# Performance work log

Measured on AMD Instinct MI355X. Metric: run time of the kernel, lower is better.

The kernel has to match this reference:

```python
import jax, jax.numpy as jnp
import numpy as np

DROPOUT_P = 0.0  # undefined global `dropout_p` in source; pinned to 0 (identity) for determinism


def setup_inputs() -> dict:
    key = jax.random.key(0)
    k1, k2, k3 = jax.random.split(key, 3)
    B, Lq, Lk, D = 16, 4096, 4096, 64
    return {
        "query": jax.random.normal(k1, (B, Lq, D), dtype=jnp.float32),
        "key": jax.random.normal(k2, (B, Lk, D), dtype=jnp.float32),
        "value": jax.random.normal(k3, (B, Lk, D), dtype=jnp.float32),
        "scale_factor": jnp.ones((1,), dtype=jnp.float32),
    }


def reference(query, key, value, scale_factor):
    # scores: [B, Lq, Lk] -- the large HBM-materialized intermediate
    scores = jnp.einsum("bqd,bkd->bqk", query, key) / scale_factor
    probs = jax.nn.softmax(scores, axis=-1)
    # dropout with p = DROPOUT_P = 0.0 is the identity
    out = jnp.einsum("bqk,bkd->bqd", probs, value)
    return out
```

## Files before the change

### kernel.cpp

```cpp
#include <hip/hip_runtime.h>
#include <hip/hip_fp16.h>

typedef _Float16 half2_t __attribute__((ext_vector_type(2)));
typedef _Float16 half4_t __attribute__((ext_vector_type(4)));
typedef _Float16 half8_t __attribute__((ext_vector_type(8)));
typedef float   float4_t __attribute__((ext_vector_type(4)));
typedef float  float16_t __attribute__((ext_vector_type(16)));

static __device__ __forceinline__ half2_t cvt_pk(float a, float b) {
    return __builtin_bit_cast(half2_t, __builtin_amdgcn_cvt_pkrtz(a, b));
}
static __device__ __forceinline__ half4_t cvt_pk4(float a, float b, float c, float d) {
    half2_t lo = cvt_pk(a, b), hi = cvt_pk(c, d);
    half4_t r;
    r[0] = lo[0]; r[1] = lo[1]; r[2] = hi[0]; r[3] = hi[1];
    return r;
}
static __device__ __forceinline__ half8_t cvt_pk8(const float4& a, const float4& b) {
    half4_t lo = cvt_pk4(a.x, a.y, a.z, a.w);
    half4_t hi = cvt_pk4(b.x, b.y, b.z, b.w);
    return __builtin_shufflevector(lo, hi, 0, 1, 2, 3, 4, 5, 6, 7);
}
static __device__ __forceinline__ half8_t join8(half4_t lo, half4_t hi) {
    return __builtin_shufflevector(lo, hi, 0, 1, 2, 3, 4, 5, 6, 7);
}
static __device__ __forceinline__ float f3(float a, float b, float c) {
    return fmaxf(fmaxf(a, b), c);
}

namespace {
constexpr int kB       = 16;
constexpr int kL       = 4096;
constexpr int kD       = 64;
constexpr int kQTile   = 128;
constexpr int kBK      = 64;
constexpr int kTiles   = kL / kBK;
constexpr int kSplit   = 2;
constexpr int kTilesHf = kTiles / kSplit;
constexpr int kTileH   = kBK * kD;
constexpr int kKStride = 72;
constexpr size_t kWsHalves = (size_t)kB * kTiles * kTileH;
constexpr size_t kOHalves  = (size_t)kB * kL * kD;
}


__global__ __launch_bounds__(256) void prep_kv(const float* __restrict__ K,
                                               const float* __restrict__ V,
                                               _Float16* __restrict__ Kws,
                                               _Float16* __restrict__ Vws)
{
    int blk = blockIdx.x;
    const int tid = threadIdx.x;
    if (blk < kB * kTiles) {
        const float* src = K + (size_t)blk * kTileH;
        _Float16* dst = Kws + (size_t)blk * kTileH;
#pragma unroll
        for (int i = 0; i < 2; ++i) {
            const int task = tid + 256 * i;
            const int row  = task >> 3;
            const int g    = task & 7;
            const int srow = (row & ~12) | ((row & 4) << 1) | ((row & 8) >> 1);
            const float* p = src + srow * kD + g * 8;
            const float4 a  = *(const float4*)p;
            const float4 b2 = *(const float4*)(p + 4);
            *(half8_t*)(dst + task * 8) = cvt_pk8(a, b2);
        }
    } else {
        blk -= kB * kTiles;
        const float* src = V + (size_t)blk * kTileH;
        _Float16* dst = Vws + (size_t)blk * kTileH;
        const int d  = tid & 63;
        const int vw = tid >> 6;
#pragma unroll
        for (int i = 0; i < 2; ++i) {
            const int c8 = vw * 2 + i;
            const int k0 = c8 * 8;
            float p[8];
#pragma unroll
            for (int j = 0; j < 8; ++j) p[j] = src[(k0 + j) * kD + d];
            half4_t lo = cvt_pk4(p[0], p[1], p[2], p[3]);
            half4_t hi = cvt_pk4(p[4], p[5], p[6], p[7]);
            *(half8_t*)(dst + (c8 * 64 + d) * 8) = join8(lo, hi);
        }
    }
}

__global__ __launch_bounds__(256, 4)
void fa_fwd(const float* __restrict__ Q, const _Float16* __restrict__ Kws,
            const _Float16* __restrict__ Vws, const float* __restrict__ scale_ptr,
            float* __restrict__ Out, _Float16* __restrict__ O2ws,
            float* __restrict__ Mlws)
{
    __shared__ __align__(16) _Float16 Ksh[2][kBK * kKStride];

    const int tid  = threadIdx.x;
    const int wave = tid >> 6;
    const int lane = tid & 63;
    const int l31  = lane & 31;
    const int hi   = lane >> 5;

    const int b  = blockIdx.y;
    const int hf = blockIdx.z;
    const int q0 = blockIdx.x * kQTile + wave * 32;

    const int task0 = tid, task1 = tid + 256;
    const int koff0 = (task0 >> 3) * kKStride + (task0 & 7) * 8;
    const int koff1 = (task1 >> 3) * kKStride + (task1 & 7) * 8;

    const float qscale = 1.4426950408889634f / scale_ptr[0];

    const float*    Qb = Q   + (size_t)b * kL * kD;
    const _Float16* Kt = Kws + ((size_t)b * kTiles + (size_t)hf * kTilesHf) * kTileH;
    const _Float16* Vt = Vws + ((size_t)b * kTiles + (size_t)hf * kTilesHf) * kTileH;

    half8_t qfrag[4];
    {
        const float* qrow = Qb + (size_t)(q0 + l31) * kD;
#pragma unroll
        for (int kd = 0; kd < 4; ++kd) {
            const float* p = qrow + kd * 16 + hi * 8;
            half8_t h;
#pragma unroll
            for (int j = 0; j < 8; ++j) h[j] = (_Float16)(p[j] * qscale);
            qfrag[kd] = h;
        }
    }

    float16_t O[2];
    O[0] = (float16_t)0.0f;
    O[1] = (float16_t)0.0f;
    float m_run = -__builtin_inff();
    float l_run = 0.0f;
    const float16_t Zc = (float16_t)0.0f;

    half8_t kp[2];
    kp[0] = *(const half8_t*)(Kt + task0 * 8);
    kp[1] = *(const half8_t*)(Kt + task1 * 8);
    *(half8_t*)(&Ksh[0][koff0]) = kp[0];
    *(half8_t*)(&Ksh[0][koff1]) = kp[1];
    kp[0] = *(const half8_t*)(Kt + (size_t)kTileH + task0 * 8);
    kp[1] = *(const half8_t*)(Kt + (size_t)kTileH + task1 * 8);
    __syncthreads();

    for (int t = 0; t < kTilesHf; ++t) {
        const int cur = t & 1;
        const _Float16* Kb = Ksh[cur];
        _Float16* Kn = Ksh[cur ^ 1];

        const _Float16* vtile = Vt + (size_t)t * kTileH;
        half8_t vr0[4], vr1[4];
#pragma unroll
        for (int kb = 0; kb < 4; ++kb) {
            const _Float16* pch = vtile + (kb * 2 + hi) * 512;
            vr0[kb] = *(const half8_t*)(pch + l31 * 8);
            vr1[kb] = *(const half8_t*)(pch + (32 + l31) * 8);
        }

        float16_t S0, S1;
        {
            half8_t kf0, kf1;
            kf0 = *(const half8_t*)(&Kb[(l31)      * kKStride + 0 * 16 + hi * 8]);
            kf1 = *(const half8_t*)(&Kb[(32 + l31) * kKStride + 0 * 16 + hi * 8]);
            __builtin_amdgcn_s_setprio(1);
            S0 = __builtin_amdgcn_mfma_f32_32x32x16_f16(kf0, qfrag[0], Zc, 0, 0, 0);
            S1 = __builtin_amdgcn_mfma_f32_32x32x16_f16(kf1, qfrag[0], Zc, 0, 0, 0);
#pragma unroll
            for (int kd = 1; kd < 4; ++kd) {
                kf0 = *(const half8_t*)(&Kb[(l31)      * kKStride + kd * 16 + hi * 8]);
                kf1 = *(const half8_t*)(&Kb[(32 + l31) * kKStride + kd * 16 + hi * 8]);
                S0 = __builtin_amdgcn_mfma_f32_32x32x16_f16(kf0, qfrag[kd], S0, 0, 0, 0);
                S1 = __builtin_amdgcn_mfma_f32_32x32x16_f16(kf1, qfrag[kd], S1, 0, 0, 0);
            }
            __builtin_amdgcn_s_setprio(0);
        }

        *(half8_t*)(&Kn[koff0]) = kp[0];
        *(half8_t*)(&Kn[koff1]) = kp[1];
        {
            const int nt = (t + 2) & (kTilesHf - 1);
            const _Float16* kn = Kt + (size_t)nt * kTileH;
            kp[0] = *(const half8_t*)(kn + task0 * 8);
            kp[1] = *(const half8_t*)(kn + task1 * 8);
        }

        float v0 = f3(S0[0],  S0[1],  S0[2]);
        float v1 = f3(S0[3],  S0[4],  S0[5]);
        float v2 = f3(S0[6],  S0[7],  S0[8]);
        float v3 = f3(S0[9],  S0[10], S0[11]);
        float v4 = f3(S0[12], S0[13], S0[14]);
        float v5 = f3(S0[15], S1[0],  S1[1]);
        float v6 = f3(S1[2],  S1[3],  S1[4]);
        float v7 = f3(S1[5],  S1[6],  S1[7]);
        float v8 = f3(S1[8],  S1[9],  S1[10]);
        float v9 = f3(S1[11], S1[12], S1[13]);
        float w0 = f3(v0, v1, v2);
        float w1 = f3(v3, v4, v5);
        float w2 = f3(v6, v7, v8);
        float w3 = f3(v9, S1[14], S1[15]);
        float pm = fmaxf(fmaxf(w0, w1), fmaxf(w2, w3));
        pm = fmaxf(pm, __shfl_xor(pm, 32));

        const bool need = pm > m_run + 8.0f;
        if (__ballot(need)) {
            const float mn    = fmaxf(m_run, pm);
            const float alpha = __builtin_amdgcn_exp2f(m_run - mn);
            m_run = mn;
            l_run *= alpha;
#pragma unroll
            for (int r = 0; r < 16; ++r) { O[0][r] *= alpha; O[1][r] *= alpha; }
        }

#pragma unroll
        for (int r = 0; r < 16; ++r) {
            S0[r] = __builtin_amdgcn_exp2f(S0[r] - m_run);
            S1[r] = __builtin_amdgcn_exp2f(S1[r] - m_run);
        }
        half8_t pf[4];
        pf[0] = join8(cvt_pk4(S0[0],  S0[1],  S0[2],  S0[3]),
                      cvt_pk4(S0[4],  S0[5],  S0[6],  S0[7]));
        pf[1] = join8(cvt_pk4(S0[8],  S0[9],  S0[10], S0[11]),
                      cvt_pk4(S0[12], S0[13], S0[14], S0[15]));
        pf[2] = join8(cvt_pk4(S1[0],  S1[1],  S1[2],  S1[3]),
                      cvt_pk4(S1[4],  S1[5],  S1[6],  S1[7]));
        pf[3] = join8(cvt_pk4(S1[8],  S1[9],  S1[10], S1[11]),
                      cvt_pk4(S1[12], S1[13], S1[14], S1[15]));
#define A4(v,a) ((v[a] + v[(a)+1]) + (v[(a)+2] + v[(a)+3]))
        l_run += ((A4(S0, 0) + A4(S0, 4)) + (A4(S0, 8) + A4(S0, 12)))
               + ((A4(S1, 0) + A4(S1, 4)) + (A4(S1, 8) + A4(S1, 12)));
#undef A4

        __builtin_amdgcn_s_setprio(1);
#pragma unroll
        for (int kb = 0; kb < 4; ++kb) {
            O[0] = __builtin_amdgcn_mfma_f32_32x32x16_f16(vr0[kb], pf[kb], O[0], 0, 0, 0);
            O[1] = __builtin_amdgcn_mfma_f32_32x32x16_f16(vr1[kb], pf[kb], O[1], 0, 0, 0);
        }
        __builtin_amdgcn_s_setprio(0);

        __syncthreads();
    }

    l_run += __shfl_xor(l_run, 32);
    const float inv = 1.0f / l_run;
    const int   q   = q0 + l31;
    if (hf == 0) {
        float* op = Out + ((size_t)b * kL + q) * kD;
#pragma unroll
        for (int dt = 0; dt < 2; ++dt)
#pragma unroll
            for (int rr = 0; rr < 4; ++rr) {
                const int d0 = dt * 32 + rr * 8 + hi * 4;
                float4 w;
                w.x = O[dt][rr * 4 + 0] * inv;
                w.y = O[dt][rr * 4 + 1] * inv;
                w.z = O[dt][rr * 4 + 2] * inv;
                w.w = O[dt][rr * 4 + 3] * inv;
                *(float4*)(op + d0) = w;
            }
    } else {
        _Float16* op = O2ws + ((size_t)b * kL + q) * kD;
#pragma unroll
        for (int dt = 0; dt < 2; ++dt)
#pragma unroll
            for (int rr = 0; rr < 4; ++rr) {
                const int d0 = dt * 32 + rr * 8 + hi * 4;
                half4_t w = cvt_pk4(O[dt][rr * 4 + 0] * inv, O[dt][rr * 4 + 1] * inv,
                                    O[dt][rr * 4 + 2] * inv, O[dt][rr * 4 + 3] * inv);
                *(half4_t*)(op + d0) = w;
            }
    }
    if (hi == 0) {
        float2 ml; ml.x = m_run; ml.y = l_run;
        *(float2*)(Mlws + (((size_t)b * kL + q) * 2 + hf) * 2) = ml;
    }
}

__global__ __launch_bounds__(256)
void combine(float* __restrict__ Out, const _Float16* __restrict__ O2ws,
             const float* __restrict__ Mlws)
{
    const int t   = threadIdx.x;
    const int row = blockIdx.x * 16 + (t >> 4);
    const int d0  = (t & 15) * 4;

    const float m1 = Mlws[(size_t)row * 4 + 0];
    const float l1 = Mlws[(size_t)row * 4 + 1];
    const float m2 = Mlws[(size_t)row * 4 + 2];
    const float l2 = Mlws[(size_t)row * 4 + 3];

    const float m  = fmaxf(m1, m2);
    float w1 = l1 * exp2f(m1 - m);
    float w2 = l2 * exp2f(m2 - m);
    const float inv = 1.0f / (w1 + w2);
    w1 *= inv; w2 *= inv;

    float* op = Out + (size_t)row * kD + d0;
    const _Float16* o2 = O2ws + (size_t)row * kD + d0;
    float4 a = *(const float4*)op;
    const half4_t h = *(const half4_t*)o2;
    a.x = a.x * w1 + (float)h[0] * w2;
    a.y = a.y * w1 + (float)h[1] * w2;
    a.z = a.z * w1 + (float)h[2] * w2;
    a.w = a.w * w1 + (float)h[3] * w2;
    *(float4*)op = a;
}

extern "C" void kernel_launch(void* const* d_in, const int* in_sizes, int n_in,
                              void* d_out, int out_size, void* d_ws, size_t ws_size,
                              hipStream_t stream) {
    const float* Q = (const float*)d_in[0];
    const float* K = (const float*)d_in[1];
    const float* V = (const float*)d_in[2];
    const float* s = (const float*)d_in[3];
    float* out = (float*)d_out;
    _Float16* Kws  = (_Float16*)d_ws;
    _Float16* Vws  = Kws + kWsHalves;
    _Float16* O2ws = Vws + kWsHalves;
    float*    Mlws = (float*)(O2ws + kOHalves);

    prep_kv<<<dim3(2 * kB * kTiles), dim3(256), 0, stream>>>(K, V, Kws, Vws);
    fa_fwd<<<dim3(kL / kQTile, kB, kSplit), dim3(256), 0, stream>>>(Q, Kws, Vws, s, out, O2ws, Mlws);
    combine<<<dim3(kB * kL / 16), dim3(256), 0, stream>>>(out, O2ws, Mlws);
}
```

Measured before the change: 231.4 us.

## Stage K and V tiles into LDS via direct global-to-LDS loads with XOR swizzle

Replaces the register-staged, padded K shared buffer with direct global_load_lds copies of both K and V tiles into a double-buffered shared region. The prep kernel now writes K with an XOR swizzle on 8-element groups, so unpadded LDS reads avoid bank conflicts. V fragments are read from shared memory instead of straight from global into registers. This aims to cut register pressure and VMEM-to-register traffic, and to overlap next-tile loads with compute. In exchange it doubles LDS use, which may lower occupancy, and the prefetch is issued one tile ahead instead of two.

```diff
diff --git a/kernel.cpp b/kernel.cpp
--- a/kernel.cpp
+++ b/kernel.cpp
@@ -26,6 +26,12 @@
 }
 static __device__ __forceinline__ float f3(float a, float b, float c) {
     return fmaxf(fmaxf(a, b), c);
+}
+
+static __device__ __forceinline__ void stage16(const _Float16* g, _Float16* l) {
+    __builtin_amdgcn_global_load_lds(
+        (const __attribute__((address_space(1))) char*)(const void*)g,
+        (__attribute__((address_space(3))) char*)(void*)l, 16, 0, 0);
 }
 
 namespace {
@@ -38,7 +44,7 @@
 constexpr int kSplit   = 2;
 constexpr int kTilesHf = kTiles / kSplit;
 constexpr int kTileH   = kBK * kD;
-constexpr int kKStride = 72;
+constexpr int kBufH    = 2 * kTileH;
 constexpr size_t kWsHalves = (size_t)kB * kTiles * kTileH;
 constexpr size_t kOHalves  = (size_t)kB * kL * kD;
 }
@@ -58,9 +64,10 @@
         for (int i = 0; i < 2; ++i) {
             const int task = tid + 256 * i;
             const int row  = task >> 3;
-            const int g    = task & 7;
+            const int gp   = task & 7;
             const int srow = (row & ~12) | ((row & 4) << 1) | ((row & 8) >> 1);
-            const float* p = src + srow * kD + g * 8;
+            const int glog = gp ^ (row & 7);
+            const float* p = src + srow * kD + glog * 8;
             const float4 a  = *(const float4*)p;
             const float4 b2 = *(const float4*)(p + 4);
             *(half8_t*)(dst + task * 8) = cvt_pk8(a, b2);
@@ -91,7 +98,7 @@
             float* __restrict__ Out, _Float16* __restrict__ O2ws,
             float* __restrict__ Mlws)
 {
-    __shared__ __align__(16) _Float16 Ksh[2][kBK * kKStride];
+    __shared__ __align__(16) _Float16 SH[2 * kBufH];
 
     const int tid  = threadIdx.x;
     const int wave = tid >> 6;
@@ -103,15 +110,20 @@
     const int hf = blockIdx.z;
     const int q0 = blockIdx.x * kQTile + wave * 32;
 
-    const int task0 = tid, task1 = tid + 256;
-    const int koff0 = (task0 >> 3) * kKStride + (task0 & 7) * 8;
-    const int koff1 = (task1 >> 3) * kKStride + (task1 & 7) * 8;
-
     const float qscale = 1.4426950408889634f / scale_ptr[0];
 
     const float*    Qb = Q   + (size_t)b * kL * kD;
     const _Float16* Kt = Kws + ((size_t)b * kTiles + (size_t)hf * kTilesHf) * kTileH;
     const _Float16* Vt = Vws + ((size_t)b * kTiles + (size_t)hf * kTilesHf) * kTileH;
+
+    const int rs = l31 & 7;
+    int ka[4];
+#pragma unroll
+    for (int kd = 0; kd < 4; ++kd)
+        ka[kd] = l31 * 64 + (((kd * 2 + hi) ^ rs) << 3);
+    const int va = kTileH + hi * 512 + l31 * 8;
+
+    const int sdst = wave * 512;
 
     half8_t qfrag[4];
     {
@@ -133,54 +145,49 @@
     float l_run = 0.0f;
     const float16_t Zc = (float16_t)0.0f;
 
-    half8_t kp[2];
-    kp[0] = *(const half8_t*)(Kt + task0 * 8);
-    kp[1] = *(const half8_t*)(Kt + task1 * 8);
-    *(half8_t*)(&Ksh[0][koff0]) = kp[0];
-    *(half8_t*)(&Ksh[0][koff1]) = kp[1];
-    kp[0] = *(const half8_t*)(Kt + (size_t)kTileH + task0 * 8);
-    kp[1] = *(const half8_t*)(Kt + (size_t)kTileH + task1 * 8);
+    stage16(Kt + tid * 8,                SH + sdst);
+    stage16(Kt + (tid + 256) * 8,        SH + 2048 + sdst);
+    stage16(Vt + tid * 8,                SH + kTileH + sdst);
+    stage16(Vt + (tid + 256) * 8,        SH + kTileH + 2048 + sdst);
     __syncthreads();
 
     for (int t = 0; t < kTilesHf; ++t) {
-        const int cur = t & 1;
-        const _Float16* Kb = Ksh[cur];
-        _Float16* Kn = Ksh[cur ^ 1];
-
-        const _Float16* vtile = Vt + (size_t)t * kTileH;
-        half8_t vr0[4], vr1[4];
-#pragma unroll
-        for (int kb = 0; kb < 4; ++kb) {
-            const _Float16* pch = vtile + (kb * 2 + hi) * 512;
-            vr0[kb] = *(const half8_t*)(pch + l31 * 8);
-            vr1[kb] = *(const half8_t*)(pch + (32 + l31) * 8);
+        const int cb = (t & 1) * kBufH;
+        const int nb = ((t + 1) & 1) * kBufH;
+
+        {
+            const int nt = (t + 1) & (kTilesHf - 1);
+            const _Float16* kg = Kt + (size_t)nt * kTileH;
+            const _Float16* vg = Vt + (size_t)nt * kTileH;
+            stage16(kg + tid * 8,         SH + nb + sdst);
+            stage16(kg + (tid + 256) * 8, SH + nb + 2048 + sdst);
+            stage16(vg + tid * 8,         SH + nb + kTileH + sdst);
+            stage16(vg + (tid + 256) * 8, SH + nb + kTileH + 2048 + sdst);
         }
 
         float16_t S0, S1;
         {
             half8_t kf0, kf1;
-            kf0 = *(const half8_t*)(&Kb[(l31)      * kKStride + 0 * 16 + hi * 8]);
-            kf1 = *(const half8_t*)(&Kb[(32 + l31) * kKStride + 0 * 16 + hi * 8]);
+            kf0 = *(const half8_t*)(&SH[cb + ka[0]]);
+            kf1 = *(const half8_t*)(&SH[cb + ka[0] + 2048]);
             __builtin_amdgcn_s_setprio(1);
             S0 = __builtin_amdgcn_mfma_f32_32x32x16_f16(kf0, qfrag[0], Zc, 0, 0, 0);
             S1 = __builtin_amdgcn_mfma_f32_32x32x16_f16(kf1, qfrag[0], Zc, 0, 0, 0);
 #pragma unroll
             for (int kd = 1; kd < 4; ++kd) {
-                kf0 = *(const half8_t*)(&Kb[(l31)      * kKStride + kd * 16 + hi * 8]);
-                kf1 = *(const half8_t*)(&Kb[(32 + l31) * kKStride + kd * 16 + hi * 8]);
+                kf0 = *(const half8_t*)(&SH[cb + ka[kd]]);
+                kf1 = *(const half8_t*)(&SH[cb + ka[kd] + 2048]);
                 S0 = __builtin_amdgcn_mfma_f32_32x32x16_f16(kf0, qfrag[kd], S0, 0, 0, 0);
                 S1 = __builtin_amdgcn_mfma_f32_32x32x16_f16(kf1, qfrag[kd], S1, 0, 0, 0);
             }
             __builtin_amdgcn_s_setprio(0);
         }
 
-        *(half8_t*)(&Kn[koff0]) = kp[0];
-        *(half8_t*)(&Kn[koff1]) = kp[1];
-        {
-            const int nt = (t + 2) & (kTilesHf - 1);
-            const _Float16* kn = Kt + (size_t)nt * kTileH;
-            kp[0] = *(const half8_t*)(kn + task0 * 8);
-            kp[1] = *(const half8_t*)(kn + task1 * 8);
+        half8_t vf0[4], vf1[4];
+#pragma unroll
+        for (int kb = 0; kb < 4; ++kb) {
+            vf0[kb] = *(const half8_t*)(&SH[cb + va + kb * 1024]);
+            vf1[kb] = *(const half8_t*)(&SH[cb + va + kb * 1024 + 256]);
         }
 
         float v0 = f3(S0[0],  S0[1],  S0[2]);
@@ -232,8 +239,8 @@
         __builtin_amdgcn_s_setprio(1);
 #pragma unroll
         for (int kb = 0; kb < 4; ++kb) {
-            O[0] = __builtin_amdgcn_mfma_f32_32x32x16_f16(vr0[kb], pf[kb], O[0], 0, 0, 0);
-            O[1] = __builtin_amdgcn_mfma_f32_32x32x16_f16(vr1[kb], pf[kb], O[1], 0, 0, 0);
+            O[0] = __builtin_amdgcn_mfma_f32_32x32x16_f16(vf0[kb], pf[kb], O[0], 0, 0, 0);
+            O[1] = __builtin_amdgcn_mfma_f32_32x32x16_f16(vf1[kb], pf[kb], O[1], 0, 0, 0);
         }
         __builtin_amdgcn_s_setprio(0);
 
```

Result: faster. 197.6 us (-14.6%).
